# Performance work log

Measured on AMD Instinct MI355X. Metric: run time of the kernel, lower is better.

The kernel has to match this reference:

```python
import jax, jax.numpy as jnp
import numpy as np

DIM = 1024
NUM_HEADS = 16
HEAD_DIM = DIM // NUM_HEADS
TAU = 1.0
LAMBDA_JUMP = 0.6
LAMBDA_LOCAL = 0.4
MIN_ENTROPY = 0.5
WINDOW = 3
EPS = 1e-10


def local_diffusion_kernel(seq_len, strength, window=WINDOW):
    # Banded Gaussian kernel, row-normalized. [S, S]
    i = jnp.arange(seq_len)
    d = i[:, None] - i[None, :]
    k = jnp.where(jnp.abs(d) <= window,
                  jnp.exp(-(d.astype(jnp.float32) ** 2) / (2.0 * strength ** 2)),
                  0.0)
    return k / (k.sum(axis=-1, keepdims=True) + EPS)


def setup_inputs() -> dict:
    key = jax.random.key(0)
    ks = jax.random.split(key, 9)
    scale = 0.02
    x = jax.random.normal(ks[0], (2, 2048, DIM), dtype=jnp.float32)
    Wq = jax.random.normal(ks[1], (DIM, DIM), dtype=jnp.float32) * scale
    bq = jax.random.normal(ks[2], (DIM,), dtype=jnp.float32) * scale
    Wk = jax.random.normal(ks[3], (DIM, DIM), dtype=jnp.float32) * scale
    bk = jax.random.normal(ks[4], (DIM,), dtype=jnp.float32) * scale
    Wv = jax.random.normal(ks[5], (DIM, DIM), dtype=jnp.float32) * scale
    bv = jax.random.normal(ks[6], (DIM,), dtype=jnp.float32) * scale
    Wo = jax.random.normal(ks[7], (DIM, DIM), dtype=jnp.float32) * scale
    bo = jax.random.normal(ks[8], (DIM,), dtype=jnp.float32) * scale
    return {"x": x, "Wq": Wq, "bq": bq, "Wk": Wk, "bk": bk,
            "Wv": Wv, "bv": bv, "Wo": Wo, "bo": bo}


def reference(x, Wq, bq, Wk, bk, Wv, bv, Wo, bo):
    B, S, D = x.shape
    H, hd = NUM_HEADS, HEAD_DIM
    # torch Linear: y = x @ W.T + b
    Q = (x @ Wq.T + bq).reshape(B, S, H, hd).transpose(0, 2, 1, 3)  # [B,H,S,hd]
    K = (x @ Wk.T + bk).reshape(B, S, H, hd).transpose(0, 2, 1, 3)
    V = (x @ Wv.T + bv).reshape(B, S, H, hd).transpose(0, 2, 1, 3)

    scores = jnp.einsum('bhqd,bhkd->bhqk', Q, K) / (TAU * np.sqrt(hd).astype(np.float32))
    A = jax.nn.softmax(scores, axis=-1)  # [B,H,S,S]

    # Per-row entropy gating (detach-based in torch: forward value is unchanged)
    entropy = -jnp.sum(A * jnp.log(A + EPS), axis=-1, keepdims=True)
    stable = jax.lax.stop_gradient((entropy >= MIN_ENTROPY).astype(A.dtype))
    A = stable * A + (1.0 - stable) * jax.lax.stop_gradient(A)

    L = local_diffusion_kernel(S, LAMBDA_LOCAL)  # [S,S]
    A_stable = LAMBDA_JUMP * A + (1.0 - LAMBDA_JUMP) * L[None, None, :, :]

    out = jnp.einsum('bhqk,bhkd->bhqd', A_stable, V)  # [B,H,S,hd]
    out = out.transpose(0, 2, 1, 3).reshape(B, S, D)
    return out @ Wo.T + bo
```

## Files before the change

kernel.cpp:

```cpp
#include <hip/hip_runtime.h>
#include <math.h>

typedef __bf16 bf16x8 __attribute__((ext_vector_type(8)));
typedef float f32x4 __attribute__((ext_vector_type(4)));

namespace {
constexpr int DIMC = 1024, NH = 16, HD = 64, SEQ = 2048;
constexpr float SCL2 = 0.1803368801f;
}

__device__ __forceinline__ unsigned short f2b(float f) {
  unsigned u = __float_as_uint(f);
  return (unsigned short)((u + 0x7fffu + ((u >> 16) & 1u)) >> 16);
}
__device__ __forceinline__ float b2f(unsigned short s) {
  return __uint_as_float((unsigned)s << 16);
}
__device__ __forceinline__ unsigned cvtpk(float lo, float hi) {
  unsigned r;
  asm("v_cvt_pk_bf16_f32 %0, %1, %2" : "=v"(r) : "v"(lo), "v"(hi));
  return r;
}
__device__ __forceinline__ void gld16(void* l, const void* g) {
  __builtin_amdgcn_global_load_lds(
      (const __attribute__((address_space(1))) void*)g,
      (__attribute__((address_space(3))) void*)l, 16, 0, 0);
}

#define TBAR() do {                                                        \
  asm volatile("s_waitcnt vmcnt(3) lgkmcnt(0)\n\ts_barrier" ::: "memory"); \
  __builtin_amdgcn_sched_barrier(0);                                       \
} while (0)

__global__ __launch_bounds__(256)
void cvt_all(const float* __restrict__ x,
             const float* __restrict__ w0, const float* __restrict__ w1,
             const float* __restrict__ w2, const float* __restrict__ w3,
             unsigned short* __restrict__ xb, unsigned short* __restrict__ wb) {
  const int bid = blockIdx.x;
  const float* src;
  unsigned short* dst;
  int i;
  if (bid < 2048) {
    src = x; dst = xb; i = bid * 256 + threadIdx.x;
  } else {
    const int r = (bid - 2048) >> 9, lb = (bid - 2048) & 511;
    src = r == 0 ? w0 : r == 1 ? w1 : r == 2 ? w2 : w3;
    dst = wb + (size_t)r * 1048576;
    i = lb * 256 + threadIdx.x;
  }
  const float4* in4 = (const float4*)src;
  float4 a = in4[2 * i], b = in4[2 * i + 1];
  union { unsigned short u[8]; uint4 v; } r;
  r.u[0] = f2b(a.x); r.u[1] = f2b(a.y); r.u[2] = f2b(a.z); r.u[3] = f2b(a.w);
  r.u[4] = f2b(b.x); r.u[5] = f2b(b.y); r.u[6] = f2b(b.z); r.u[7] = f2b(b.w);
  ((uint4*)dst)[i] = r.v;
}

template<int MODE>
__device__ __forceinline__
void gemm_tile128(const unsigned short* __restrict__ A, const unsigned short* __restrict__ W,
                  const float* __restrict__ bias, void* __restrict__ Cout,
                  int bm, int bn, float scl, bool kswz, char* As, char* Bs) {
  const int tid = threadIdx.x, lane = tid & 63, w = tid >> 6;
  const int p = lane & 15, g = lane >> 4;
  const int wr = w >> 1, wc = w & 1;
  const int sr = tid >> 2, sc = (tid & 3) * 8;

  f32x4 acc[4][4];
#pragma unroll
  for (int mf = 0; mf < 4; ++mf)
#pragma unroll
    for (int nf = 0; nf < 4; ++nf)
      acc[mf][nf] = (f32x4){0.f, 0.f, 0.f, 0.f};

  const size_t arow0 = (size_t)(bm + sr) * DIMC + sc;
  const size_t arow1 = (size_t)(bm + 64 + sr) * DIMC + sc;
  const size_t brow0 = (size_t)(bn + sr) * DIMC + sc;
  const size_t brow1 = (size_t)(bn + 64 + sr) * DIMC + sc;

  for (int k0 = 0; k0 < DIMC; k0 += 32) {
    __syncthreads();
    gld16(&As[tid * 16],        &A[arow0 + k0]);
    gld16(&As[4096 + tid * 16], &A[arow1 + k0]);
    gld16(&Bs[tid * 16],        &W[brow0 + k0]);
    gld16(&Bs[4096 + tid * 16], &W[brow1 + k0]);
    __syncthreads();
    bf16x8 af[4], bfr[4];
#pragma unroll
    for (int mf = 0; mf < 4; ++mf)
      af[mf] = *(const bf16x8*)&As[(wr * 64 + mf * 16 + p) * 64 + g * 16];
#pragma unroll
    for (int nf = 0; nf < 4; ++nf)
      bfr[nf] = *(const bf16x8*)&Bs[(wc * 64 + nf * 16 + p) * 64 + g * 16];
#pragma unroll
    for (int mf = 0; mf < 4; ++mf)
#pragma unroll
      for (int nf = 0; nf < 4; ++nf)
        acc[mf][nf] = __builtin_amdgcn_mfma_f32_16x16x32_bf16(af[mf], bfr[nf], acc[mf][nf], 0, 0, 0);
  }

#pragma unroll
  for (int nf = 0; nf < 4; ++nf) {
    const int cg = bn + wc * 64 + nf * 16 + p;
    const float bv = bias[cg & (DIMC - 1)];
#pragma unroll
    for (int mf = 0; mf < 4; ++mf) {
#pragma unroll
      for (int j = 0; j < 4; ++j) {
        const int rg = bm + wr * 64 + mf * 16 + g * 4 + j;
        const float v = (acc[mf][nf][j] + bv) * scl;
        if (MODE == 0) {
          ((float*)Cout)[(size_t)rg * DIMC + cg] = v;
        } else {
          const int bb = rg >> 11, ss = rg & (SEQ - 1);
          const int hh = cg >> 6;
          int dd = cg & (HD - 1);
          if (kswz) dd ^= (ss & 7) << 3;
          ((unsigned short*)Cout)[(((size_t)(bb * NH + hh) * SEQ + ss) * HD) + dd] = f2b(v);
        }
      }
    }
  }
}

__global__ __launch_bounds__(256, 2)
void gemm_qkv(const unsigned short* __restrict__ A, const unsigned short* __restrict__ Wall,
              const float* __restrict__ bq, const float* __restrict__ bk,
              const float* __restrict__ bv, unsigned short* __restrict__ Out) {
  __shared__ char As[8192];
  __shared__ char Bs[8192];
  const int which = blockIdx.z;
  const unsigned short* W = Wall + (size_t)which * 1048576;
  const float* bias = which == 0 ? bq : which == 1 ? bk : bv;
  unsigned short* Cout = Out + (size_t)which * 4194304;
  const float scl = which == 0 ? SCL2 : 1.0f;
  gemm_tile128<1>(A, W, bias, Cout, blockIdx.x * 128, blockIdx.y * 128, scl, which == 1, As, Bs);
}

__global__ __launch_bounds__(256, 2)
void gemm_out(const unsigned short* __restrict__ A, const unsigned short* __restrict__ W,
              const float* __restrict__ bias, float* __restrict__ Cout) {
  __shared__ char As[8192];
  __shared__ char Bs[4096];
  const int tid = threadIdx.x, lane = tid & 63, w = tid >> 6;
  const int p = lane & 15, g = lane >> 4;
  const int wr = w >> 1, wc = w & 1;
  const int bm = blockIdx.x * 128, bn = blockIdx.y * 64;
  const int sr = tid >> 2, sc = (tid & 3) * 8;

  f32x4 acc[4][2];
#pragma unroll
  for (int mf = 0; mf < 4; ++mf)
#pragma unroll
    for (int nf = 0; nf < 2; ++nf)
      acc[mf][nf] = (f32x4){0.f, 0.f, 0.f, 0.f};

  const size_t arow0 = (size_t)(bm + sr) * DIMC + sc;
  const size_t arow1 = (size_t)(bm + 64 + sr) * DIMC + sc;
  const size_t brow  = (size_t)(bn + sr) * DIMC + sc;

  for (int k0 = 0; k0 < DIMC; k0 += 32) {
    __syncthreads();
    gld16(&As[tid * 16],        &A[arow0 + k0]);
    gld16(&As[4096 + tid * 16], &A[arow1 + k0]);
    gld16(&Bs[tid * 16],        &W[brow + k0]);
    __syncthreads();
    bf16x8 af[4], bfr[2];
#pragma unroll
    for (int mf = 0; mf < 4; ++mf)
      af[mf] = *(const bf16x8*)&As[(wr * 64 + mf * 16 + p) * 64 + g * 16];
#pragma unroll
    for (int nf = 0; nf < 2; ++nf)
      bfr[nf] = *(const bf16x8*)&Bs[(wc * 32 + nf * 16 + p) * 64 + g * 16];
#pragma unroll
    for (int mf = 0; mf < 4; ++mf)
#pragma unroll
      for (int nf = 0; nf < 2; ++nf)
        acc[mf][nf] = __builtin_amdgcn_mfma_f32_16x16x32_bf16(af[mf], bfr[nf], acc[mf][nf], 0, 0, 0);
  }

#pragma unroll
  for (int nf = 0; nf < 2; ++nf) {
    const int cg = bn + wc * 32 + nf * 16 + p;
    const float bv = bias[cg];
#pragma unroll
    for (int mf = 0; mf < 4; ++mf) {
#pragma unroll
      for (int j = 0; j < 4; ++j) {
        const int rg = bm + wr * 64 + mf * 16 + g * 4 + j;
        Cout[(size_t)rg * DIMC + cg] = acc[mf][nf][j] + bv;
      }
    }
  }
}

__global__ __launch_bounds__(512, 4)
void attn_fused(const unsigned short* __restrict__ Q, const unsigned short* __restrict__ K,
                const unsigned short* __restrict__ V, unsigned short* __restrict__ Y) {
  __shared__ char Kl[3][8192];
  __shared__ char Vt[2][8192];
  __shared__ char Pl[16384];
  const int tid = threadIdx.x, lane = tid & 63, w = tid >> 6;
  const int p = lane & 15, g = lane >> 4;
  const int bh = blockIdx.x, b = bh >> 4, h = bh & 15;
  const int q0 = blockIdx.y * 128;
  const int qwv = q0 + w * 16;
  const size_t base = (size_t)bh * SEQ * HD;
  const unsigned short* Qp = Q + base;
  const unsigned short* Vp = V + base;

  union Vu { bf16x8 v; unsigned short u[8]; };

  bf16x8 qf[2];
#pragma unroll
  for (int ks = 0; ks < 2; ++ks)
    qf[ks] = *(const bf16x8*)&Qp[(size_t)(qwv + p) * HD + ks * 32 + g * 8];

  bf16x8 ones8;
  {
    union { unsigned short u[8]; bf16x8 v; } o;
#pragma unroll
    for (int e = 0; e < 8; ++e) o.u[e] = (p == 0) ? (unsigned short)0x3F80 : (unsigned short)0;
    ones8 = o.v;
  }

  const unsigned short* kSrc = K + base + (size_t)(tid >> 3) * HD + (tid & 7) * 8;
  const int kp = tid & 31, vd0 = ((tid >> 5) & 7) * 8;
  const bool vload = tid < 256;
  const unsigned short* vSrc = Vp + (size_t)(2 * kp) * HD + vd0;

  const int swz = (p & 7) << 4;
  int sCol[2], pwCol[4], colE[8];
#pragma unroll
  for (int ks = 0; ks < 2; ++ks) sCol[ks] = (ks * 64 + g * 16) ^ swz;
#pragma unroll
  for (int nf = 0; nf < 4; ++nf) pwCol[nf] = (nf * 32 + g * 8) ^ swz;
#pragma unroll
  for (int e = 0; e < 8; ++e) colE[e] = (kp * 4) ^ (e << 4);

  f32x4 o2[4];
  f32x4 ol;
#pragma unroll
  for (int nf = 0; nf < 4; ++nf) o2[nf] = (f32x4){0.f, 0.f, 0.f, 0.f};
  ol = (f32x4){0.f, 0.f, 0.f, 0.f};

  Vu v0A, v1A, v0B, v1B;

  auto gldK = [&](int par, int kb) {
    gld16(&Kl[par][tid * 16], kSrc + (size_t)kb * HD);
  };
  auto loadV = [&](Vu& a0, Vu& a1, int kb) {
    if (vload) {
      a0.v = *(const bf16x8*)(vSrc + (size_t)kb * HD);
      a1.v = *(const bf16x8*)(vSrc + (size_t)(kb + 1) * HD);
    }
  };
  auto writeV = [&](int par, Vu& a0, Vu& a1) {
    if (vload) {
      char* vtp = &Vt[par][0] + vd0 * 128;
#pragma unroll
      for (int e = 0; e < 8; ++e) {
        const unsigned val = (unsigned)a0.u[e] | ((unsigned)a1.u[e] << 16);
        *(unsigned*)(vtp + e * 128 + colE[e]) = val;
      }
    }
  };
  auto qkt_sm_stage = [&](int kpar) {
    const char* klp = &Kl[kpar][0] + p * 128;
    bf16x8 kf[4][2];
#pragma unroll
    for (int nf = 0; nf < 4; ++nf)
#pragma unroll
      for (int ks = 0; ks < 2; ++ks)
        kf[nf][ks] = *(const bf16x8*)(klp + nf * 2048 + sCol[ks]);
    f32x4 s[4];
#pragma unroll
    for (int nf = 0; nf < 4; ++nf) s[nf] = (f32x4){0.f, 0.f, 0.f, 0.f};
    __builtin_amdgcn_s_setprio(1);
#pragma unroll
    for (int nf = 0; nf < 4; ++nf)
#pragma unroll
      for (int ks = 0; ks < 2; ++ks)
        s[nf] = __builtin_amdgcn_mfma_f32_16x16x32_bf16(kf[nf][ks], qf[ks], s[nf], 0, 0, 0);
    __builtin_amdgcn_s_setprio(0);
#pragma unroll
    for (int nf = 0; nf < 4; ++nf)
#pragma unroll
      for (int j = 0; j < 4; ++j)
        s[nf][j] = exp2f(s[nf][j]);
    char* plp = &Pl[0] + w * 2048 + p * 128;
#pragma unroll
    for (int nf = 0; nf < 4; ++nf) {
      uint2 val;
      val.x = cvtpk(s[nf][0], s[nf][1]);
      val.y = cvtpk(s[nf][2], s[nf][3]);
      *(uint2*)(plp + pwCol[nf]) = val;
    }
  };
  auto pv = [&](int vpar) {
    const char* plp = &Pl[0] + w * 2048 + p * 128;
    bf16x8 pf[2];
#pragma unroll
    for (int ks = 0; ks < 2; ++ks)
      pf[ks] = *(const bf16x8*)(plp + sCol[ks]);
    const char* vtp = &Vt[vpar][0] + p * 128;
    bf16x8 vb[4][2];
#pragma unroll
    for (int nfd = 0; nfd < 4; ++nfd)
#pragma unroll
      for (int ks = 0; ks < 2; ++ks)
        vb[nfd][ks] = *(const bf16x8*)(vtp + nfd * 2048 + sCol[ks]);
    __builtin_amdgcn_s_setprio(1);
#pragma unroll
    for (int nfd = 0; nfd < 4; ++nfd)
#pragma unroll
      for (int ks = 0; ks < 2; ++ks)
        o2[nfd] = __builtin_amdgcn_mfma_f32_16x16x32_bf16(vb[nfd][ks], pf[ks], o2[nfd], 0, 0, 0);
#pragma unroll
    for (int ks = 0; ks < 2; ++ks)
      ol = __builtin_amdgcn_mfma_f32_16x16x32_bf16(ones8, pf[ks], ol, 0, 0, 0);
    __builtin_amdgcn_s_setprio(0);
  };

  gldK(0, 0);
  gldK(1, 64);
  loadV(v0A, v1A, 0);
  __syncthreads();

  for (int it = 0; it < 5; ++it) {
    const int t0 = it * 6;
    gldK(2, (t0 + 2) * 64); loadV(v0B, v1B, (t0 + 1) * 64);
    qkt_sm_stage(0); writeV(0, v0A, v1A); TBAR(); pv(0);

    gldK(0, (t0 + 3) * 64); loadV(v0A, v1A, (t0 + 2) * 64);
    qkt_sm_stage(1); writeV(1, v0B, v1B); TBAR(); pv(1);

    gldK(1, (t0 + 4) * 64); loadV(v0B, v1B, (t0 + 3) * 64);
    qkt_sm_stage(2); writeV(0, v0A, v1A); TBAR(); pv(0);

    gldK(2, (t0 + 5) * 64); loadV(v0A, v1A, (t0 + 4) * 64);
    qkt_sm_stage(0); writeV(1, v0B, v1B); TBAR(); pv(1);

    gldK(0, (t0 + 6) * 64); loadV(v0B, v1B, (t0 + 5) * 64);
    qkt_sm_stage(1); writeV(0, v0A, v1A); TBAR(); pv(0);

    gldK(1, (t0 + 7) * 64); loadV(v0A, v1A, (t0 + 6) * 64);
    qkt_sm_stage(2); writeV(1, v0B, v1B); TBAR(); pv(1);
  }
  loadV(v0B, v1B, 31 * 64);
  qkt_sm_stage(0); writeV(0, v0A, v1A); TBAR(); pv(0);
  qkt_sm_stage(1); writeV(1, v0B, v1B); TBAR(); pv(1);

  const float e1 = 4.3936934e-2f, e2 = 3.7266532e-6f, e3 = 6.1019804e-13f;
  const float lwv[4] = {1.f, e1, e2, e3};
  {
    const int q = qwv + p;
    const float lq = __shfl(ol[0], p);
    const float inv = 0.6f / lq;
    float wsum = 0.f;
#pragma unroll
    for (int dd = -3; dd <= 3; ++dd) {
      const int kk = q + dd;
      if (kk >= 0 && kk < SEQ) wsum += lwv[dd < 0 ? -dd : dd];
    }
    const float wn = 0.4f / (wsum + 1e-10f);
#pragma unroll
    for (int nfd = 0; nfd < 4; ++nfd) {
      const int d0 = nfd * 16 + g * 4;
      float loc[4] = {0.f, 0.f, 0.f, 0.f};
#pragma unroll
      for (int dd = -3; dd <= 3; ++dd) {
        const int kk = q + dd;
        if (kk >= 0 && kk < SEQ) {
          const uint2 lv = *(const uint2*)&Vp[(size_t)kk * HD + d0];
          const float wt = lwv[dd < 0 ? -dd : dd];
          loc[0] = fmaf(wt, b2f((unsigned short)lv.x), loc[0]);
          loc[1] = fmaf(wt, b2f((unsigned short)(lv.x >> 16)), loc[1]);
          loc[2] = fmaf(wt, b2f((unsigned short)lv.y), loc[2]);
          loc[3] = fmaf(wt, b2f((unsigned short)(lv.y >> 16)), loc[3]);
        }
      }
      uint2 st;
      st.x = cvtpk(o2[nfd][0] * inv + loc[0] * wn, o2[nfd][1] * inv + loc[1] * wn);
      st.y = cvtpk(o2[nfd][2] * inv + loc[2] * wn, o2[nfd][3] * inv + loc[3] * wn);
      *(uint2*)&Y[((size_t)(b * SEQ + q)) * DIMC + h * HD + d0] = st;
    }
  }
}

extern "C" void kernel_launch(void* const* d_in, const int* in_sizes, int n_in,
                              void* d_out, int out_size, void* d_ws, size_t ws_size,
                              hipStream_t stream) {
  (void)in_sizes; (void)n_in; (void)out_size; (void)ws_size;
  const float* x  = (const float*)d_in[0];
  const float* Wq = (const float*)d_in[1];
  const float* bq = (const float*)d_in[2];
  const float* Wk = (const float*)d_in[3];
  const float* bk = (const float*)d_in[4];
  const float* Wv = (const float*)d_in[5];
  const float* bv = (const float*)d_in[6];
  const float* Wo = (const float*)d_in[7];
  const float* bo = (const float*)d_in[8];

  char* ws = (char*)d_ws;
  unsigned short* xb  = (unsigned short*)(ws);
  unsigned short* Wqb = (unsigned short*)(ws + 8388608);
  unsigned short* Wob = (unsigned short*)(ws + 14680064);
  unsigned short* Qh  = (unsigned short*)(ws + 16777216);
  unsigned short* Kh  = (unsigned short*)(ws + 25165824);
  unsigned short* Vh  = (unsigned short*)(ws + 33554432);
  unsigned short* Yb  = (unsigned short*)(ws + 41943040);

  dim3 blk(256);
  cvt_all<<<4096, blk, 0, stream>>>(x, Wq, Wk, Wv, Wo, xb, Wqb);

  gemm_qkv<<<dim3(32, 8, 3), blk, 0, stream>>>(xb, Wqb, bq, bk, bv, Qh);

  attn_fused<<<dim3(32, 16), dim3(512), 0, stream>>>(Qh, Kh, Vh, Yb);

  gemm_out<<<dim3(32, 16), blk, 0, stream>>>(Yb, Wob, bo, (float*)d_out);
}
```

Baseline: 127.0 us.

## Halve attention block to 256 threads with two query tiles per wave

Result: slower. 131.7 us (+3.7%).

```diff
diff --git a/kernel.cpp b/kernel.cpp
--- a/kernel.cpp
+++ b/kernel.cpp
@@ -28,7 +28,7 @@
 }
 
 #define TBAR() do {                                                        \
-  asm volatile("s_waitcnt vmcnt(3) lgkmcnt(0)\n\ts_barrier" ::: "memory"); \
+  asm volatile("s_waitcnt vmcnt(4) lgkmcnt(0)\n\ts_barrier" ::: "memory"); \
   __builtin_amdgcn_sched_barrier(0);                                       \
 } while (0)
 
@@ -195,7 +195,7 @@
   }
 }
 
-__global__ __launch_bounds__(512, 4)
+__global__ __launch_bounds__(256, 2)
 void attn_fused(const unsigned short* __restrict__ Q, const unsigned short* __restrict__ K,
                 const unsigned short* __restrict__ V, unsigned short* __restrict__ Y) {
   __shared__ char Kl[3][8192];
@@ -205,17 +205,19 @@
   const int p = lane & 15, g = lane >> 4;
   const int bh = blockIdx.x, b = bh >> 4, h = bh & 15;
   const int q0 = blockIdx.y * 128;
-  const int qwv = q0 + w * 16;
+  const int qwv = q0 + w * 32;
   const size_t base = (size_t)bh * SEQ * HD;
   const unsigned short* Qp = Q + base;
   const unsigned short* Vp = V + base;
 
   union Vu { bf16x8 v; unsigned short u[8]; };
 
-  bf16x8 qf[2];
-#pragma unroll
-  for (int ks = 0; ks < 2; ++ks)
-    qf[ks] = *(const bf16x8*)&Qp[(size_t)(qwv + p) * HD + ks * 32 + g * 8];
+  bf16x8 qf[2][2];
+#pragma unroll
+  for (int mi = 0; mi < 2; ++mi)
+#pragma unroll
+    for (int ks = 0; ks < 2; ++ks)
+      qf[mi][ks] = *(const bf16x8*)&Qp[(size_t)(qwv + mi * 16 + p) * HD + ks * 32 + g * 8];
 
   bf16x8 ones8;
   {
@@ -227,7 +229,6 @@
 
   const unsigned short* kSrc = K + base + (size_t)(tid >> 3) * HD + (tid & 7) * 8;
   const int kp = tid & 31, vd0 = ((tid >> 5) & 7) * 8;
-  const bool vload = tid < 256;
   const unsigned short* vSrc = Vp + (size_t)(2 * kp) * HD + vd0;
 
   const int swz = (p & 7) << 4;
@@ -239,31 +240,31 @@
 #pragma unroll
   for (int e = 0; e < 8; ++e) colE[e] = (kp * 4) ^ (e << 4);
 
-  f32x4 o2[4];
-  f32x4 ol;
-#pragma unroll
-  for (int nf = 0; nf < 4; ++nf) o2[nf] = (f32x4){0.f, 0.f, 0.f, 0.f};
-  ol = (f32x4){0.f, 0.f, 0.f, 0.f};
+  f32x4 o2[2][4];
+  f32x4 ol[2];
+#pragma unroll
+  for (int mi = 0; mi < 2; ++mi) {
+#pragma unroll
+    for (int nf = 0; nf < 4; ++nf) o2[mi][nf] = (f32x4){0.f, 0.f, 0.f, 0.f};
+    ol[mi] = (f32x4){0.f, 0.f, 0.f, 0.f};
+  }
 
   Vu v0A, v1A, v0B, v1B;
 
   auto gldK = [&](int par, int kb) {
-    gld16(&Kl[par][tid * 16], kSrc + (size_t)kb * HD);
+    gld16(&Kl[par][tid * 16],        kSrc + (size_t)kb * HD);
+    gld16(&Kl[par][4096 + tid * 16], kSrc + (size_t)(kb + 32) * HD);
   };
   auto loadV = [&](Vu& a0, Vu& a1, int kb) {
-    if (vload) {
-      a0.v = *(const bf16x8*)(vSrc + (size_t)kb * HD);
-      a1.v = *(const bf16x8*)(vSrc + (size_t)(kb + 1) * HD);
-    }
+    a0.v = *(const bf16x8*)(vSrc + (size_t)kb * HD);
+    a1.v = *(const bf16x8*)(vSrc + (size_t)(kb + 1) * HD);
   };
   auto writeV = [&](int par, Vu& a0, Vu& a1) {
-    if (vload) {
-      char* vtp = &Vt[par][0] + vd0 * 128;
-#pragma unroll
-      for (int e = 0; e < 8; ++e) {
-        const unsigned val = (unsigned)a0.u[e] | ((unsigned)a1.u[e] << 16);
-        *(unsigned*)(vtp + e * 128 + colE[e]) = val;
-      }
+    char* vtp = &Vt[par][0] + vd0 * 128;
+#pragma unroll
+    for (int e = 0; e < 8; ++e) {
+      const unsigned val = (unsigned)a0.u[e] | ((unsigned)a1.u[e] << 16);
+      *(unsigned*)(vtp + e * 128 + colE[e]) = val;
     }
   };
   auto qkt_sm_stage = [&](int kpar) {
@@ -274,36 +275,34 @@
 #pragma unroll
       for (int ks = 0; ks < 2; ++ks)
         kf[nf][ks] = *(const bf16x8*)(klp + nf * 2048 + sCol[ks]);
-    f32x4 s[4];
-#pragma unroll
-    for (int nf = 0; nf < 4; ++nf) s[nf] = (f32x4){0.f, 0.f, 0.f, 0.f};
-    __builtin_amdgcn_s_setprio(1);
-#pragma unroll
-    for (int nf = 0; nf < 4; ++nf)
-#pragma unroll
-      for (int ks = 0; ks < 2; ++ks)
-        s[nf] = __builtin_amdgcn_mfma_f32_16x16x32_bf16(kf[nf][ks], qf[ks], s[nf], 0, 0, 0);
-    __builtin_amdgcn_s_setprio(0);
-#pragma unroll
-    for (int nf = 0; nf < 4; ++nf)
-#pragma unroll
-      for (int j = 0; j < 4; ++j)
-        s[nf][j] = exp2f(s[nf][j]);
-    char* plp = &Pl[0] + w * 2048 + p * 128;
-#pragma unroll
-    for (int nf = 0; nf < 4; ++nf) {
-      uint2 val;
-      val.x = cvtpk(s[nf][0], s[nf][1]);
-      val.y = cvtpk(s[nf][2], s[nf][3]);
-      *(uint2*)(plp + pwCol[nf]) = val;
+#pragma unroll
+    for (int mi = 0; mi < 2; ++mi) {
+      f32x4 s[4];
+#pragma unroll
+      for (int nf = 0; nf < 4; ++nf) s[nf] = (f32x4){0.f, 0.f, 0.f, 0.f};
+      __builtin_amdgcn_s_setprio(1);
+#pragma unroll
+      for (int nf = 0; nf < 4; ++nf)
+#pragma unroll
+        for (int ks = 0; ks < 2; ++ks)
+          s[nf] = __builtin_amdgcn_mfma_f32_16x16x32_bf16(kf[nf][ks], qf[mi][ks], s[nf], 0, 0, 0);
+      __builtin_amdgcn_s_setprio(0);
+#pragma unroll
+      for (int nf = 0; nf < 4; ++nf)
+#pragma unroll
+        for (int j = 0; j < 4; ++j)
+          s[nf][j] = exp2f(s[nf][j]);
+      char* plp = &Pl[0] + w * 4096 + mi * 2048 + p * 128;
+#pragma unroll
+      for (int nf = 0; nf < 4; ++nf) {
+        uint2 val;
+        val.x = cvtpk(s[nf][0], s[nf][1]);
+        val.y = cvtpk(s[nf][2], s[nf][3]);
+        *(uint2*)(plp + pwCol[nf]) = val;
+      }
     }
   };
   auto pv = [&](int vpar) {
-    const char* plp = &Pl[0] + w * 2048 + p * 128;
-    bf16x8 pf[2];
-#pragma unroll
-    for (int ks = 0; ks < 2; ++ks)
-      pf[ks] = *(const bf16x8*)(plp + sCol[ks]);
     const char* vtp = &Vt[vpar][0] + p * 128;
     bf16x8 vb[4][2];
 #pragma unroll
@@ -311,16 +310,24 @@
 #pragma unroll
       for (int ks = 0; ks < 2; ++ks)
         vb[nfd][ks] = *(const bf16x8*)(vtp + nfd * 2048 + sCol[ks]);
-    __builtin_amdgcn_s_setprio(1);
-#pragma unroll
-    for (int nfd = 0; nfd < 4; ++nfd)
+#pragma unroll
+    for (int mi = 0; mi < 2; ++mi) {
+      const char* plp = &Pl[0] + w * 4096 + mi * 2048 + p * 128;
+      bf16x8 pf[2];
 #pragma unroll
       for (int ks = 0; ks < 2; ++ks)
-        o2[nfd] = __builtin_amdgcn_mfma_f32_16x16x32_bf16(vb[nfd][ks], pf[ks], o2[nfd], 0, 0, 0);
-#pragma unroll
-    for (int ks = 0; ks < 2; ++ks)
-      ol = __builtin_amdgcn_mfma_f32_16x16x32_bf16(ones8, pf[ks], ol, 0, 0, 0);
-    __builtin_amdgcn_s_setprio(0);
+        pf[ks] = *(const bf16x8*)(plp + sCol[ks]);
+      __builtin_amdgcn_s_setprio(1);
+#pragma unroll
+      for (int nfd = 0; nfd < 4; ++nfd)
+#pragma unroll
+        for (int ks = 0; ks < 2; ++ks)
+          o2[mi][nfd] = __builtin_amdgcn_mfma_f32_16x16x32_bf16(vb[nfd][ks], pf[ks], o2[mi][nfd], 0, 0, 0);
+#pragma unroll
+      for (int ks = 0; ks < 2; ++ks)
+        ol[mi] = __builtin_amdgcn_mfma_f32_16x16x32_bf16(ones8, pf[ks], ol[mi], 0, 0, 0);
+      __builtin_amdgcn_s_setprio(0);
+    }
   };
 
   gldK(0, 0);
@@ -354,9 +361,10 @@
 
   const float e1 = 4.3936934e-2f, e2 = 3.7266532e-6f, e3 = 6.1019804e-13f;
   const float lwv[4] = {1.f, e1, e2, e3};
-  {
-    const int q = qwv + p;
-    const float lq = __shfl(ol[0], p);
+#pragma unroll
+  for (int mi = 0; mi < 2; ++mi) {
+    const int q = qwv + mi * 16 + p;
+    const float lq = __shfl(ol[mi][0], p);
     const float inv = 0.6f / lq;
     float wsum = 0.f;
 #pragma unroll
@@ -382,8 +390,8 @@
         }
       }
       uint2 st;
-      st.x = cvtpk(o2[nfd][0] * inv + loc[0] * wn, o2[nfd][1] * inv + loc[1] * wn);
-      st.y = cvtpk(o2[nfd][2] * inv + loc[2] * wn, o2[nfd][3] * inv + loc[3] * wn);
+      st.x = cvtpk(o2[mi][nfd][0] * inv + loc[0] * wn, o2[mi][nfd][1] * inv + loc[1] * wn);
+      st.y = cvtpk(o2[mi][nfd][2] * inv + loc[2] * wn, o2[mi][nfd][3] * inv + loc[3] * wn);
       *(uint2*)&Y[((size_t)(b * SEQ + q)) * DIMC + h * HD + d0] = st;
     }
   }
@@ -417,7 +425,7 @@
 
   gemm_qkv<<<dim3(32, 8, 3), blk, 0, stream>>>(xb, Wqb, bq, bk, bv, Qh);
 
-  attn_fused<<<dim3(32, 16), dim3(512), 0, stream>>>(Qh, Kh, Vh, Yb);
+  attn_fused<<<dim3(32, 16), blk, 0, stream>>>(Qh, Kh, Vh, Yb);
 
   gemm_out<<<dim3(32, 16), blk, 0, stream>>>(Yb, Wob, bo, (float*)d_out);
 }
```
